# Optimization experiments

Hardware: AMD Instinct MI355X
Metric: run time of the kernel (lower is better)

Reference implementation:

```python
import jax, jax.numpy as jnp
import numpy as np

N = 4096       # number of nodes
IN = 256       # in_features
OUT = 128      # out_features
EDGE = 5       # edge feature dim = IN + 5 - 2*OUT
SLOPE = 0.2    # LeakyReLU negative slope (alpha)
NEG = -9.0e15  # masking constant from original code


def setup_inputs() -> dict:
    key = jax.random.key(0)
    k1, k2, k3, k4 = jax.random.split(key, 4)
    ids = jnp.arange(N, dtype=jnp.int64) if jax.config.jax_enable_x64 else jnp.arange(N, dtype=jnp.int32)
    lstm_out = jax.random.normal(k1, (N, IN), dtype=jnp.float32)
    edges_list = jax.random.normal(k2, (N * N, EDGE), dtype=jnp.float32)
    # xavier_uniform-like scale for W and a (gain 1.414)
    w_scale = 1.414 * jnp.sqrt(2.0 / (IN + OUT))
    a_scale = 1.414 * jnp.sqrt(2.0 / (IN + 5 + 1))
    W = jax.random.normal(k3, (IN, OUT), dtype=jnp.float32) * w_scale
    a = jax.random.normal(k4, (IN + 5, 1), dtype=jnp.float32) * a_scale
    return {"ids": ids, "lstm_out": lstm_out, "edges_list": edges_list,
            "W": W, "a": a, "first": 1}


def reference(ids, lstm_out, edges_list, W, a, first):
    # ids are unique (arange), so the dict-based segment-mean is the identity:
    # hij == lstm_out in original-row order.
    n = lstm_out.shape[0]
    wh = lstm_out @ W  # [n, OUT]
    # Additive score decomposed into three partial dot products instead of
    # materializing the [n*n, IN+5] concatenated tensor:
    # a = [a_i (OUT), a_e (EDGE), a_j (OUT)]
    a_i = a[:OUT, 0]
    a_e = a[OUT:OUT + EDGE, 0]
    a_j = a[OUT + EDGE:, 0]
    s_i = wh @ a_i                               # [n]
    s_j = wh @ a_j                               # [n]
    s_e = (edges_list @ a_e).reshape(n, n)       # [n, n], row-major (i, j)
    scores = jax.nn.leaky_relu(s_i[:, None] + s_e + s_j[None, :], SLOPE)
    # adjacency = all-ones with zero diagonal -> mask the diagonal
    mask = ~jnp.eye(n, dtype=bool)
    scores = jnp.where(mask, scores, jnp.float32(NEG))
    attention = jax.nn.softmax(scores, axis=1)   # dropout is eval no-op
    alpha = attention @ wh                       # [n, OUT]
    return alpha
```

## Files before the change

kernel.cpp:

```cpp
#include <hip/hip_runtime.h>
#include <hip/hip_bf16.h>

#define N 4096
#define IND 256
#define OUTD 128
#define NEGV -9000000000000000.0f

typedef __attribute__((ext_vector_type(8))) short bf16x8;
typedef __attribute__((ext_vector_type(4))) float f32x4;

static __device__ __forceinline__ unsigned short f2bf(float x) {
    unsigned int u = __float_as_uint(x);
    u = (u + 0x7FFFu + ((u >> 16) & 1u)) >> 16;
    return (unsigned short)u;
}

__global__ __launch_bounds__(256) void wh_kernel(const float* __restrict__ x,
                                                 const float* __restrict__ W,
                                                 float* __restrict__ wh) {
    __shared__ float xs[8][IND];
    const int t = threadIdx.x;
    const int i0 = blockIdx.x * 8;
    const float4* src = (const float4*)(x + (size_t)i0 * IND);
    float4* dst = (float4*)&xs[0][0];
    dst[t] = src[t];
    dst[t + 256] = src[t + 256];
    __syncthreads();
    const int c = t & 127;
    const int rbase = (t >> 7) * 4;
    float acc[4] = {0.f, 0.f, 0.f, 0.f};
    #pragma unroll 4
    for (int k = 0; k < IND; k += 4) {
        const float w0 = W[(k + 0) * OUTD + c];
        const float w1 = W[(k + 1) * OUTD + c];
        const float w2 = W[(k + 2) * OUTD + c];
        const float w3 = W[(k + 3) * OUTD + c];
        #pragma unroll
        for (int r = 0; r < 4; ++r) {
            const float4 xv = *(const float4*)&xs[rbase + r][k];
            acc[r] = fmaf(xv.x, w0, acc[r]);
            acc[r] = fmaf(xv.y, w1, acc[r]);
            acc[r] = fmaf(xv.z, w2, acc[r]);
            acc[r] = fmaf(xv.w, w3, acc[r]);
        }
    }
    #pragma unroll
    for (int r = 0; r < 4; ++r)
        wh[(size_t)(i0 + rbase + r) * OUTD + c] = acc[r];
}

__global__ __launch_bounds__(128) void sij_kernel(const float* __restrict__ wh,
                                                  const float* __restrict__ a,
                                                  float* __restrict__ s_i,
                                                  float* __restrict__ s_j) {
    const int i = blockIdx.x;
    const int c = threadIdx.x;
    float v = wh[(size_t)i * OUTD + c];
    float p = v * a[c];
    float q = v * a[OUTD + 5 + c];
    #pragma unroll
    for (int off = 32; off >= 1; off >>= 1) {
        p += __shfl_down(p, off);
        q += __shfl_down(q, off);
    }
    __shared__ float tmp[4];
    if ((c & 63) == 0) { tmp[c >> 6] = p; tmp[2 + (c >> 6)] = q; }
    __syncthreads();
    if (c == 0) { s_i[i] = tmp[0] + tmp[1]; s_j[i] = tmp[2] + tmp[3]; }
}

__global__ __launch_bounds__(256) void whT_kernel(const float* __restrict__ wh,
                                                  unsigned short* __restrict__ whT) {
    __shared__ float ls[64][130];
    const int t = threadIdx.x;
    const int j0 = blockIdx.x * 64;
    #pragma unroll
    for (int k = 0; k < 32; ++k) {
        const int idx = k * 256 + t;
        const int j = idx >> 7;
        const int c = idx & 127;
        ls[j][c] = wh[(size_t)(j0 + j) * OUTD + c];
    }
    __syncthreads();
    #pragma unroll
    for (int k = 0; k < 32; ++k) {
        const int idx = k * 256 + t;
        const int c = idx >> 6;
        const int j = idx & 63;
        whT[(size_t)c * N + j0 + j] = f2bf(ls[j][c]);
    }
}

#define BI 16
#define BJ 64
#define NCH 4
#define CHJ (N / NCH)
#define NSUB (CHJ / BJ)
#define PPAD 72
#define EFLOATS (BI * BJ * 5)

__device__ __forceinline__ void gload_lds16(const void* g, void* l) {
    __builtin_amdgcn_global_load_lds(
        (const __attribute__((address_space(1))) unsigned int*)(g),
        (__attribute__((address_space(3))) unsigned int*)(l),
        16, 0, 0);
}

__global__ __launch_bounds__(256, 1) void gat_mfma(const float* __restrict__ edges,
                                                   const unsigned short* __restrict__ whT,
                                                   const float* __restrict__ s_iv,
                                                   const float* __restrict__ s_jv,
                                                   const float* __restrict__ a,
                                                   float* __restrict__ part,
                                                   float* __restrict__ lout) {
    __shared__ float E[2][EFLOATS];
    __shared__ unsigned short P[2][BI * PPAD];

    const int t = threadIdx.x;
    const int ib = blockIdx.x & 255;
    const int ch = blockIdx.x >> 8;
    const int i0 = ib * BI;
    const int jbase = ch * CHJ;
    const int w = t >> 6;
    const int s = t & 63;
    const int lhi = s >> 4;
    const int llo = s & 15;

    const float ae0 = a[OUTD + 0], ae1 = a[OUTD + 1], ae2 = a[OUTD + 2],
                ae3 = a[OUTD + 3], ae4 = a[OUTD + 4];
    float si[4];
    #pragma unroll
    for (int rr = 0; rr < 4; ++rr) si[rr] = s_iv[i0 + 4 * w + rr];

    const char* g0; const char* g1; const char* g2; const char* g3; const char* g4;
    {
        const char* eb = (const char*)edges + (size_t)jbase * 20;
        #define MKG(K, VAR)                                                    \
        {   const int f = K * 256 + t;                                         \
            const int row = f / 80;                                            \
            const int rem = f - row * 80;                                      \
            VAR = eb + (size_t)(i0 + row) * (N * 20) + (size_t)rem * 16; }
        MKG(0, g0) MKG(1, g1) MKG(2, g2) MKG(3, g3) MKG(4, g4)
        #undef MKG
    }
    #define STAGE(BB, ST)                                                      \
    {   const size_t jo = (size_t)(ST) * (BJ * 20);                            \
        gload_lds16(g0 + jo, &E[BB][(0 * 256 + t) * 4]);                       \
        gload_lds16(g1 + jo, &E[BB][(1 * 256 + t) * 4]);                       \
        gload_lds16(g2 + jo, &E[BB][(2 * 256 + t) * 4]);                       \
        gload_lds16(g3 + jo, &E[BB][(3 * 256 + t) * 4]);                       \
        gload_lds16(g4 + jo, &E[BB][(4 * 256 + t) * 4]); }

    f32x4 acc0 = {0.f, 0.f, 0.f, 0.f};
    f32x4 acc1 = {0.f, 0.f, 0.f, 0.f};
    float lac[4] = {0.f, 0.f, 0.f, 0.f};

    const unsigned short* wt0 = whT + (size_t)(w * 32 + llo) * N;
    const unsigned short* wt1 = wt0 + (size_t)16 * N;

    float sj = s_jv[jbase + s];
    STAGE(0, 0)

    for (int st = 0; st < NSUB; ++st) {
        const int b = st & 1;
        const int pb = st & 1;
        const int jb = jbase + st * BJ;

        const int kof = jb + lhi * 8;
        const bf16x8 B00 = *(const bf16x8*)(wt0 + kof);
        const bf16x8 B01 = *(const bf16x8*)(wt0 + kof + 32);
        const bf16x8 B10 = *(const bf16x8*)(wt1 + kof);
        const bf16x8 B11 = *(const bf16x8*)(wt1 + kof + 32);
        float sj_nx = 0.f;
        if (st + 1 < NSUB) sj_nx = s_jv[jb + BJ + s];
        __builtin_amdgcn_sched_barrier(0);

        asm volatile("s_waitcnt vmcnt(5)" ::: "memory");
        __builtin_amdgcn_s_barrier();
        __builtin_amdgcn_sched_barrier(0);

        {
            const float* Eb = &E[b][0];
            #pragma unroll
            for (int rr = 0; rr < 4; ++rr) {
                const int row = 4 * w + rr;
                const int e = row * 320 + s * 5;
                float d = Eb[e + 4] * ae4;
                d = fmaf(Eb[e + 0], ae0, d);
                d = fmaf(Eb[e + 1], ae1, d);
                d = fmaf(Eb[e + 2], ae2, d);
                d = fmaf(Eb[e + 3], ae3, d);
                float v = si[rr] + d + sj;
                v = fmaxf(v, 0.2f * v);
                if (jb + s == i0 + row) v = NEGV;
                const float p = __expf(v);
                lac[rr] += p;
                P[pb][row * PPAD + s] = f2bf(p);
            }
        }

        if (st + 1 < NSUB) {
            STAGE(b ^ 1, st + 1)
        }

        asm volatile("s_waitcnt lgkmcnt(0)" ::: "memory");
        __builtin_amdgcn_s_barrier();
        asm volatile("" ::: "memory");

        {
            const unsigned short* Pb = &P[pb][0];
            const bf16x8 A0 = *(const bf16x8*)(Pb + llo * PPAD + lhi * 8);
            const bf16x8 A1 = *(const bf16x8*)(Pb + llo * PPAD + 32 + lhi * 8);
            acc0 = __builtin_amdgcn_mfma_f32_16x16x32_bf16(A0, B00, acc0, 0, 0, 0);
            acc1 = __builtin_amdgcn_mfma_f32_16x16x32_bf16(A0, B10, acc1, 0, 0, 0);
            acc0 = __builtin_amdgcn_mfma_f32_16x16x32_bf16(A1, B01, acc0, 0, 0, 0);
            acc1 = __builtin_amdgcn_mfma_f32_16x16x32_bf16(A1, B11, acc1, 0, 0, 0);
        }

        sj = sj_nx;
    }

    #pragma unroll
    for (int rr = 0; rr < 4; ++rr) {
        #pragma unroll
        for (int off = 32; off >= 1; off >>= 1)
            lac[rr] += __shfl_xor(lac[rr], off);
    }
    if (s == 0) {
        #pragma unroll
        for (int rr = 0; rr < 4; ++rr)
            lout[(size_t)ch * N + i0 + 4 * w + rr] = lac[rr];
    }
    #pragma unroll
    for (int reg = 0; reg < 4; ++reg) {
        const int row = lhi * 4 + reg;
        float* pr = part + ((size_t)ch * N + (i0 + row)) * OUTD + w * 32 + llo;
        pr[0]  = acc0[reg];
        pr[16] = acc1[reg];
    }
}

__global__ __launch_bounds__(256) void gat_merge(const float* __restrict__ part,
                                                 const float* __restrict__ lout,
                                                 float* __restrict__ out) {
    const int idx = blockIdx.x * 256 + threadIdx.x;
    const int i = idx >> 7;
    const float L = lout[i] + lout[N + i] + lout[2 * N + i] + lout[3 * N + i];
    const float v = part[idx] + part[(size_t)N * OUTD + idx]
                  + part[2 * (size_t)N * OUTD + idx]
                  + part[3 * (size_t)N * OUTD + idx];
    out[idx] = v / L;
}

extern "C" void kernel_launch(void* const* d_in, const int* in_sizes, int n_in,
                              void* d_out, int out_size, void* d_ws, size_t ws_size,
                              hipStream_t stream) {
    const float* lstm_out = (const float*)d_in[1];
    const float* edges    = (const float*)d_in[2];
    const float* W        = (const float*)d_in[3];
    const float* a        = (const float*)d_in[4];
    float* out = (float*)d_out;

    float* wh   = (float*)d_ws;
    float* s_i  = wh + (size_t)N * OUTD;
    float* s_j  = s_i + N;
    float* lout = s_j + N;
    float* part = lout + (size_t)NCH * N;
    unsigned short* whT = (unsigned short*)(part + (size_t)NCH * N * OUTD);

    wh_kernel<<<N / 8, 256, 0, stream>>>(lstm_out, W, wh);
    sij_kernel<<<N, 128, 0, stream>>>(wh, a, s_i, s_j);
    whT_kernel<<<N / 64, 256, 0, stream>>>(wh, whT);
    gat_mfma<<<256 * NCH, 256, 0, stream>>>(edges, whT, s_i, s_j, a, part, lout);
    gat_merge<<<(N * OUTD) / 256, 256, 0, stream>>>(part, lout, out);
}
```

Measured before the change: 101.5 us.

## Load edge features directly into registers instead of staging through LDS

The edge tile is no longer copied into LDS with async global_load_lds and double-buffered shared arrays. Each thread now loads its own 5 edge floats per row straight into registers, prefetching the next sub-tile into a second register set, with the loop unrolled by two to ping-pong between them. This drops the LDS round trip and one barrier per step. The trade-off is scalar 4-byte loads at a 20-byte stride, which may coalesce less well than the previous 16-byte transfers, plus higher register use.

```diff
diff --git a/kernel.cpp b/kernel.cpp
--- a/kernel.cpp
+++ b/kernel.cpp
@@ -97,23 +97,14 @@
 #define CHJ (N / NCH)
 #define NSUB (CHJ / BJ)
 #define PPAD 72
-#define EFLOATS (BI * BJ * 5)
-
-__device__ __forceinline__ void gload_lds16(const void* g, void* l) {
-    __builtin_amdgcn_global_load_lds(
-        (const __attribute__((address_space(1))) unsigned int*)(g),
-        (__attribute__((address_space(3))) unsigned int*)(l),
-        16, 0, 0);
-}
-
-__global__ __launch_bounds__(256, 1) void gat_mfma(const float* __restrict__ edges,
-                                                   const unsigned short* __restrict__ whT,
-                                                   const float* __restrict__ s_iv,
-                                                   const float* __restrict__ s_jv,
-                                                   const float* __restrict__ a,
-                                                   float* __restrict__ part,
-                                                   float* __restrict__ lout) {
-    __shared__ float E[2][EFLOATS];
+
+__global__ __launch_bounds__(256, 1) void gat_reg(const float* __restrict__ edges,
+                                                  const unsigned short* __restrict__ whT,
+                                                  const float* __restrict__ s_iv,
+                                                  const float* __restrict__ s_jv,
+                                                  const float* __restrict__ a,
+                                                  float* __restrict__ part,
+                                                  float* __restrict__ lout) {
     __shared__ unsigned short P[2][BI * PPAD];
 
     const int t = threadIdx.x;
@@ -132,93 +123,90 @@
     #pragma unroll
     for (int rr = 0; rr < 4; ++rr) si[rr] = s_iv[i0 + 4 * w + rr];
 
-    const char* g0; const char* g1; const char* g2; const char* g3; const char* g4;
-    {
-        const char* eb = (const char*)edges + (size_t)jbase * 20;
-        #define MKG(K, VAR)                                                    \
-        {   const int f = K * 256 + t;                                         \
-            const int row = f / 80;                                            \
-            const int rem = f - row * 80;                                      \
-            VAR = eb + (size_t)(i0 + row) * (N * 20) + (size_t)rem * 16; }
-        MKG(0, g0) MKG(1, g1) MKG(2, g2) MKG(3, g3) MKG(4, g4)
-        #undef MKG
-    }
-    #define STAGE(BB, ST)                                                      \
-    {   const size_t jo = (size_t)(ST) * (BJ * 20);                            \
-        gload_lds16(g0 + jo, &E[BB][(0 * 256 + t) * 4]);                       \
-        gload_lds16(g1 + jo, &E[BB][(1 * 256 + t) * 4]);                       \
-        gload_lds16(g2 + jo, &E[BB][(2 * 256 + t) * 4]);                       \
-        gload_lds16(g3 + jo, &E[BB][(3 * 256 + t) * 4]);                       \
-        gload_lds16(g4 + jo, &E[BB][(4 * 256 + t) * 4]); }
+    const float* er0 = edges + ((size_t)(i0 + 4 * w + 0) * N + jbase + s) * 5;
+    const float* er1 = edges + ((size_t)(i0 + 4 * w + 1) * N + jbase + s) * 5;
+    const float* er2 = edges + ((size_t)(i0 + 4 * w + 2) * N + jbase + s) * 5;
+    const float* er3 = edges + ((size_t)(i0 + 4 * w + 3) * N + jbase + s) * 5;
+
+    const unsigned short* wt0 = whT + (size_t)(w * 32 + llo) * N;
+    const unsigned short* wt1 = wt0 + (size_t)16 * N;
 
     f32x4 acc0 = {0.f, 0.f, 0.f, 0.f};
     f32x4 acc1 = {0.f, 0.f, 0.f, 0.f};
     float lac[4] = {0.f, 0.f, 0.f, 0.f};
 
-    const unsigned short* wt0 = whT + (size_t)(w * 32 + llo) * N;
-    const unsigned short* wt1 = wt0 + (size_t)16 * N;
-
+    float eA[4][5], eB[4][5];
     float sj = s_jv[jbase + s];
-    STAGE(0, 0)
-
-    for (int st = 0; st < NSUB; ++st) {
-        const int b = st & 1;
-        const int pb = st & 1;
-        const int jb = jbase + st * BJ;
-
-        const int kof = jb + lhi * 8;
-        const bf16x8 B00 = *(const bf16x8*)(wt0 + kof);
-        const bf16x8 B01 = *(const bf16x8*)(wt0 + kof + 32);
-        const bf16x8 B10 = *(const bf16x8*)(wt1 + kof);
-        const bf16x8 B11 = *(const bf16x8*)(wt1 + kof + 32);
-        float sj_nx = 0.f;
-        if (st + 1 < NSUB) sj_nx = s_jv[jb + BJ + s];
-        __builtin_amdgcn_sched_barrier(0);
-
-        asm volatile("s_waitcnt vmcnt(5)" ::: "memory");
-        __builtin_amdgcn_s_barrier();
-        __builtin_amdgcn_sched_barrier(0);
-
-        {
-            const float* Eb = &E[b][0];
-            #pragma unroll
-            for (int rr = 0; rr < 4; ++rr) {
-                const int row = 4 * w + rr;
-                const int e = row * 320 + s * 5;
-                float d = Eb[e + 4] * ae4;
-                d = fmaf(Eb[e + 0], ae0, d);
-                d = fmaf(Eb[e + 1], ae1, d);
-                d = fmaf(Eb[e + 2], ae2, d);
-                d = fmaf(Eb[e + 3], ae3, d);
-                float v = si[rr] + d + sj;
-                v = fmaxf(v, 0.2f * v);
-                if (jb + s == i0 + row) v = NEGV;
-                const float p = __expf(v);
-                lac[rr] += p;
-                P[pb][row * PPAD + s] = f2bf(p);
-            }
-        }
-
-        if (st + 1 < NSUB) {
-            STAGE(b ^ 1, st + 1)
-        }
-
-        asm volatile("s_waitcnt lgkmcnt(0)" ::: "memory");
-        __builtin_amdgcn_s_barrier();
-        asm volatile("" ::: "memory");
-
-        {
-            const unsigned short* Pb = &P[pb][0];
-            const bf16x8 A0 = *(const bf16x8*)(Pb + llo * PPAD + lhi * 8);
-            const bf16x8 A1 = *(const bf16x8*)(Pb + llo * PPAD + 32 + lhi * 8);
-            acc0 = __builtin_amdgcn_mfma_f32_16x16x32_bf16(A0, B00, acc0, 0, 0, 0);
-            acc1 = __builtin_amdgcn_mfma_f32_16x16x32_bf16(A0, B10, acc1, 0, 0, 0);
-            acc0 = __builtin_amdgcn_mfma_f32_16x16x32_bf16(A1, B01, acc0, 0, 0, 0);
-            acc1 = __builtin_amdgcn_mfma_f32_16x16x32_bf16(A1, B11, acc1, 0, 0, 0);
-        }
-
-        sj = sj_nx;
-    }
+    #pragma unroll
+    for (int k = 0; k < 5; ++k) {
+        eA[0][k] = er0[k];
+        eA[1][k] = er1[k];
+        eA[2][k] = er2[k];
+        eA[3][k] = er3[k];
+    }
+
+    #define ITER(ST, EC, EN)                                                   \
+    {                                                                          \
+        const int jb = jbase + (ST) * BJ;                                      \
+        const int pb = (ST) & 1;                                               \
+           \
+        const int kof = jb + lhi * 8;                                          \
+        const bf16x8 B00 = *(const bf16x8*)(wt0 + kof);                        \
+        const bf16x8 B01 = *(const bf16x8*)(wt0 + kof + 32);                   \
+        const bf16x8 B10 = *(const bf16x8*)(wt1 + kof);                        \
+        const bf16x8 B11 = *(const bf16x8*)(wt1 + kof + 32);                   \
+                                         \
+        float sj_nx = 0.f;                                                     \
+        if ((ST) + 1 < NSUB) {                                                 \
+            const int off = ((ST) + 1) * (BJ * 5);                             \
+            _Pragma("unroll")                                                  \
+            for (int k = 0; k < 5; ++k) {                                      \
+                EN[0][k] = er0[off + k];                                       \
+                EN[1][k] = er1[off + k];                                       \
+                EN[2][k] = er2[off + k];                                       \
+                EN[3][k] = er3[off + k];                                       \
+            }                                                                  \
+            sj_nx = s_jv[jb + BJ + s];                                         \
+        }                                                                      \
+        __builtin_amdgcn_sched_barrier(0);                                     \
+              \
+        _Pragma("unroll")                                                      \
+        for (int rr = 0; rr < 4; ++rr) {                                       \
+            const int row = 4 * w + rr;                                        \
+            float d = EC[rr][4] * ae4;                                         \
+            d = fmaf(EC[rr][0], ae0, d);                                       \
+            d = fmaf(EC[rr][1], ae1, d);                                       \
+            d = fmaf(EC[rr][2], ae2, d);                                       \
+            d = fmaf(EC[rr][3], ae3, d);                                       \
+            float v = si[rr] + d + sj;                                         \
+            v = fmaxf(v, 0.2f * v);                \
+            if (jb + s == i0 + row) v = NEGV;                                  \
+            const float p = __expf(v);                                         \
+            lac[rr] += p;                                                      \
+            P[pb][row * PPAD + s] = f2bf(p);                                   \
+        }                                                                      \
+          \
+        asm volatile("s_waitcnt lgkmcnt(0)" ::: "memory");                     \
+        __builtin_amdgcn_s_barrier();                                          \
+        asm volatile("" ::: "memory");                                         \
+                                                              \
+        {                                                                      \
+            const unsigned short* Pb = &P[pb][0];                              \
+            const bf16x8 A0 = *(const bf16x8*)(Pb + llo * PPAD + lhi * 8);     \
+            const bf16x8 A1 = *(const bf16x8*)(Pb + llo * PPAD + 32 + lhi * 8);\
+            acc0 = __builtin_amdgcn_mfma_f32_16x16x32_bf16(A0, B00, acc0, 0, 0, 0); \
+            acc1 = __builtin_amdgcn_mfma_f32_16x16x32_bf16(A0, B10, acc1, 0, 0, 0); \
+            acc0 = __builtin_amdgcn_mfma_f32_16x16x32_bf16(A1, B01, acc0, 0, 0, 0); \
+            acc1 = __builtin_amdgcn_mfma_f32_16x16x32_bf16(A1, B11, acc1, 0, 0, 0); \
+        }                                                                      \
+        sj = sj_nx;                                                            \
+    }
+
+    for (int st = 0; st < NSUB; st += 2) {
+        ITER(st, eA, eB)
+        ITER(st + 1, eB, eA)
+    }
+    #undef ITER
 
     #pragma unroll
     for (int rr = 0; rr < 4; ++rr) {
@@ -271,6 +259,6 @@
     wh_kernel<<<N / 8, 256, 0, stream>>>(lstm_out, W, wh);
     sij_kernel<<<N, 128, 0, stream>>>(wh, a, s_i, s_j);
     whT_kernel<<<N / 64, 256, 0, stream>>>(wh, whT);
-    gat_mfma<<<256 * NCH, 256, 0, stream>>>(edges, whT, s_i, s_j, a, part, lout);
+    gat_reg<<<256 * NCH, 256, 0, stream>>>(edges, whT, s_i, s_j, a, part, lout);
     gat_merge<<<(N * OUTD) / 256, 256, 0, stream>>>(part, lout, out);
 }
```

Result: faster. 99.31 us (-2.1%).
